# Optimization experiments

Measured on AMD Instinct MI355X. Metric: run time of the kernel, lower is better.

## Reference

```python
import jax, jax.numpy as jnp
import numpy as np

DIM = 1024
NUM_HEADS = 16
HEAD_DIM = DIM // NUM_HEADS
ROPE_THETA = 10000.0


def rms_norm(x, w):
    # torch nn.RMSNorm with eps=None uses finfo(dtype).eps
    eps = jnp.finfo(x.dtype).eps
    var = jnp.mean(jnp.square(x), axis=-1, keepdims=True)
    return x * jax.lax.rsqrt(var + eps) * w


def rope(x, pos, theta=ROPE_THETA):
    # x: (b, h, n, d), pos: (b, n) float positions. Rotate-half RoPE.
    d = x.shape[-1]
    inv_freq = theta ** (-jnp.arange(0, d, 2, dtype=x.dtype) / d)  # (d/2,)
    ang = pos[:, None, :, None] * inv_freq  # (b, 1, n, d/2)
    cos, sin = jnp.cos(ang), jnp.sin(ang)
    x1, x2 = jnp.split(x, 2, axis=-1)
    return jnp.concatenate([x1 * cos - x2 * sin, x1 * sin + x2 * cos], axis=-1)


def setup_inputs() -> dict:
    key = jax.random.key(0)
    ks = jax.random.split(key, 9)
    b, n = 2, 2048
    s = DIM ** -0.5
    return {
        "tgt": jax.random.normal(ks[0], (b, n, DIM), jnp.float32),
        "src": jax.random.normal(ks[1], (b, n, DIM), jnp.float32),
        "tgt_pos": jax.random.uniform(ks[2], (b, n), jnp.float32) * n,
        "src_pos": jax.random.uniform(ks[3], (b, n), jnp.float32) * n,
        "Wq": jax.random.normal(ks[4], (DIM, DIM), jnp.float32) * s,
        "Wkv": jax.random.normal(ks[5], (DIM, 2 * DIM), jnp.float32) * s,
        "Wo": jax.random.normal(ks[6], (DIM, DIM), jnp.float32) * s,
        "q_norm_w": jnp.ones((HEAD_DIM,), jnp.float32),
        "k_norm_w": jnp.ones((HEAD_DIM,), jnp.float32),
    }


def reference(tgt, src, tgt_pos, src_pos, Wq, Wkv, Wo, q_norm_w, k_norm_w):
    b, n, _ = tgt.shape
    m = src.shape[1]
    h, hd = NUM_HEADS, HEAD_DIM
    # q: (b, h, n, hd)
    q = (tgt @ Wq).reshape(b, n, h, hd).transpose(0, 2, 1, 3)
    # kv layout '(two h d)': split into k and v chunks first
    kv = (src @ Wkv).reshape(b, m, 2, h, hd)
    k = kv[:, :, 0].transpose(0, 2, 1, 3)  # (b, h, m, hd)
    v = kv[:, :, 1].transpose(0, 2, 1, 3)
    q = rms_norm(q, q_norm_w)
    k = rms_norm(k, k_norm_w)
    q = rope(q, tgt_pos)
    k = rope(k, src_pos)
    scores = jnp.einsum("bhnd,bhmd->bhnm", q, k) / (hd ** 0.5)
    attn = jax.nn.softmax(scores, axis=-1)
    x = jnp.einsum("bhnm,bhmd->bhnd", attn, v)
    x = x.transpose(0, 2, 1, 3).reshape(b, n, h * hd)
    return x @ Wo
```

## Files before the change

kernel.cpp:

```cpp
#include <hip/hip_runtime.h>
#include <hip/hip_bf16.h>
#include <stdint.h>

#define DIM 1024
#define NH 16
#define HD 64
#define BATCH 2
#define SEQ 2048
#define ROWS (BATCH*SEQ)
#define NS 2
#define CHUNK (SEQ/NS)
#define NT (CHUNK/64)

typedef __attribute__((ext_vector_type(8))) short bf16x8;
typedef __attribute__((ext_vector_type(4))) float f32x4;
typedef __attribute__((ext_vector_type(16))) float f32x16;
typedef __attribute__((ext_vector_type(4))) unsigned short u16x4;
typedef __attribute__((ext_vector_type(4))) unsigned int u32x4;

static __device__ __forceinline__ unsigned short f2bf(float f) {
    union { float f; uint32_t u; } v; v.f = f;
    uint32_t u = v.u;
    uint32_t rnd = 0x7fffu + ((u >> 16) & 1u);
    return (unsigned short)((u + rnd) >> 16);
}

static __device__ __forceinline__ unsigned cvt_pk_bf16(float lo, float hi) {
    unsigned r;
    asm("v_cvt_pk_bf16_f32 %0, %1, %2" : "=v"(r) : "v"(lo), "v"(hi));
    return r;
}

__global__ void k_pre(const float* __restrict__ tgt, const float* __restrict__ src,
                      unsigned short* __restrict__ tgt_b, unsigned short* __restrict__ src_b,
                      const float* __restrict__ Wq, const float* __restrict__ Wkv,
                      const float* __restrict__ Wo,
                      unsigned short* __restrict__ WqT, unsigned short* __restrict__ WkvT,
                      unsigned short* __restrict__ WoT) {
    __shared__ float tile[32][33];
    int blk = blockIdx.x;
    if (blk < 8192) {
        const float* in = (blk < 4096) ? tgt : src;
        unsigned short* out = (blk < 4096) ? tgt_b : src_b;
        int i = ((blk & 4095) * 256 + threadIdx.x) * 4;
        f32x4 v = *(const f32x4*)(in + i);
        u16x4 o;
        o.x = f2bf(v.x); o.y = f2bf(v.y); o.z = f2bf(v.z); o.w = f2bf(v.w);
        *(u16x4*)(out + i) = o;
        return;
    }
    int bp = blk - 8192;
    int bx = bp & 127, by = bp >> 7;
    const float* W; unsigned short* WT; int N, xb;
    if (bx < 32)      { W = Wq;  WT = WqT;  N = DIM;     xb = bx; }
    else if (bx < 96) { W = Wkv; WT = WkvT; N = 2 * DIM; xb = bx - 32; }
    else              { W = Wo;  WT = WoT;  N = DIM;     xb = bx - 96; }
    const int K = DIM;
    int nt = xb * 32, kt = by * 32;
    int x = threadIdx.x & 31, y = threadIdx.x >> 5;
    #pragma unroll
    for (int i = 0; i < 32; i += 8)
        tile[y + i][x] = W[(size_t)(kt + y + i) * N + nt + x];
    __syncthreads();
    #pragma unroll
    for (int i = 0; i < 32; i += 8)
        WT[(size_t)(nt + y + i) * K + kt + x] = f2bf(tile[x][y + i]);
}

__launch_bounds__(256, 3)
__global__ void k_gemm_qkv(const unsigned short* __restrict__ tgt_b,
                           const unsigned short* __restrict__ src_b,
                           const unsigned short* __restrict__ WqT,
                           const unsigned short* __restrict__ WkvT,
                           const float* __restrict__ tpos, const float* __restrict__ spos,
                           const float* __restrict__ qw, const float* __restrict__ kw,
                           unsigned short* __restrict__ q_a, unsigned short* __restrict__ k_f,
                           unsigned short* __restrict__ v_f) {
    __shared__ __align__(16) unsigned short As[128 * 64];
    __shared__ __align__(16) unsigned short Bs[128 * 64];
    const int tid  = threadIdx.x;
    const int wid  = tid >> 6, lane = tid & 63;
    const int l15  = lane & 15, l4 = lane >> 4;
    const int bx = blockIdx.x;
    const unsigned short* A;  const unsigned short* BT;  int n0;
    if (bx < 8) { A = tgt_b; BT = WqT;  n0 = bx * 128; }
    else        { A = src_b; BT = WkvT; n0 = (bx - 8) * 128; }
    const int K = DIM;
    const int m0 = blockIdx.y * 128;
    const int wr = wid >> 1, wc = wid & 1;
    const int srow = lane >> 3, schunk = lane & 7;

    f32x4 acc[4][4] = {};

    for (int kt = 0; kt < K; kt += 64) {
        #pragma unroll
        for (int t = 0; t < 4; ++t) {
            int r  = (t * 4 + wid) * 8 + srow;
            int ck = schunk ^ (r & 7);
            const unsigned short* ga = A  + (size_t)(m0 + r) * K + kt + ck * 8;
            const unsigned short* gb = BT + (size_t)(n0 + r) * K + kt + ck * 8;
            unsigned short* la = As + (t * 4 + wid) * 512 + lane * 8;
            unsigned short* lb = Bs + (t * 4 + wid) * 512 + lane * 8;
            __builtin_amdgcn_global_load_lds((const __attribute__((address_space(1))) void*)ga,
                                             (__attribute__((address_space(3))) void*)la, 16, 0, 0);
            __builtin_amdgcn_global_load_lds((const __attribute__((address_space(1))) void*)gb,
                                             (__attribute__((address_space(3))) void*)lb, 16, 0, 0);
        }
        __syncthreads();
        #pragma unroll
        for (int k0 = 0; k0 < 2; ++k0) {
            bf16x8 af[4], bfr[4];
            int kk = k0 * 32 + l4 * 8;
            #pragma unroll
            for (int i = 0; i < 4; ++i) {
                int ar = wr * 64 + i * 16 + l15;
                af[i]  = *(const bf16x8*)((const char*)As + ar * 128 + ((kk * 2) ^ ((ar & 7) << 4)));
                int br = wc * 64 + i * 16 + l15;
                bfr[i] = *(const bf16x8*)((const char*)Bs + br * 128 + ((kk * 2) ^ ((br & 7) << 4)));
            }
            #pragma unroll
            for (int i = 0; i < 4; ++i)
                #pragma unroll
                for (int j = 0; j < 4; ++j)
                    acc[i][j] = __builtin_amdgcn_mfma_f32_16x16x32_bf16(af[i], bfr[j], acc[i][j], 0, 0, 0);
        }
        __syncthreads();
    }

    const int colbase = n0 + wc * 64;
    const int mode = (bx < 8) ? 0 : ((colbase < 1024) ? 1 : 2);

    if (mode == 2) {
        const int h = (colbase - 1024) >> 6;
        #pragma unroll
        for (int i = 0; i < 4; ++i)
            #pragma unroll
            for (int r = 0; r < 4; ++r) {
                int row = m0 + wr * 64 + i * 16 + l4 * 4 + r;
                int b = row >> 11, mm = row & (SEQ - 1);
                int bh = b * NH + h;
                int t = mm >> 6, ks = (mm >> 5) & 1, kc = (mm >> 4) & 1;
                int hiv = (mm >> 3) & 1, e = mm & 7;
                #pragma unroll
                for (int j = 0; j < 4; ++j) {
                    int dh = j >> 1, l31v = (j & 1) * 16 + l15;
                    size_t idx = (((((size_t)(bh * 32 + t) * 2 + ks) * 2 + kc) * 2 + dh) * 2 + hiv) * 256
                                 + l31v * 8 + e;
                    v_f[idx] = f2bf(acc[i][j][r]);
                }
            }
        return;
    }

    const float* pos = (mode == 0) ? tpos : spos;
    const float* wt  = (mode == 0) ? qw : kw;
    const int h = colbase >> 6;
    const float QS = (mode == 0) ? 0.18033688011112042f : 1.0f;
    const float eps = 1.1920928955078125e-7f;

    float w4[4];
    #pragma unroll
    for (int j = 0; j < 4; ++j) w4[j] = wt[j * 16 + l15];
    float invf0 = __expf(-(float)(2 * l15) * (1.0f / 64.0f) * 9.21034037198f);
    float invf1 = __expf(-(float)(2 * (16 + l15)) * (1.0f / 64.0f) * 9.21034037198f);

    #pragma unroll
    for (int i = 0; i < 4; ++i)
        #pragma unroll
        for (int r = 0; r < 4; ++r) {
            int row = m0 + wr * 64 + i * 16 + l4 * 4 + r;
            float v0 = acc[i][0][r], v1 = acc[i][1][r], v2 = acc[i][2][r], v3 = acc[i][3][r];
            float ssq = v0 * v0 + v1 * v1 + v2 * v2 + v3 * v3;
            ssq += __shfl_xor(ssq, 1, 64);
            ssq += __shfl_xor(ssq, 2, 64);
            ssq += __shfl_xor(ssq, 4, 64);
            ssq += __shfl_xor(ssq, 8, 64);
            float sc = rsqrtf(ssq * (1.0f / 64.0f) + eps);
            v0 *= sc * w4[0]; v1 *= sc * w4[1]; v2 *= sc * w4[2]; v3 *= sc * w4[3];
            float p = pos[row];
            float s0, c0, s1, c1;
            __sincosf(p * invf0, &s0, &c0);
            __sincosf(p * invf1, &s1, &c1);
            float o0 = (v0 * c0 - v2 * s0) * QS;
            float o1 = (v1 * c1 - v3 * s1) * QS;
            float o2 = (v0 * s0 + v2 * c0) * QS;
            float o3 = (v1 * s1 + v3 * c1) * QS;
            int b = row >> 11, n = row & (SEQ - 1);
            if (mode == 0) {
                unsigned short* dst = q_a + ((size_t)(b * NH + h) * SEQ + n) * 64;
                dst[l15]      = f2bf(o0);
                dst[16 + l15] = f2bf(o1);
                dst[32 + l15] = f2bf(o2);
                dst[48 + l15] = f2bf(o3);
            } else {
                int bh = b * NH + h;
                int t = n >> 6, ksn = (n >> 5) & 1, l31k = n & 31;
                int hik = l15 >> 3, e = l15 & 7;
                size_t base = ((size_t)(bh * 32 + t) * 2 + ksn) * 4;
                k_f[(base + 0) * 512 + hik * 256 + l31k * 8 + e] = f2bf(o0);
                k_f[(base + 1) * 512 + hik * 256 + l31k * 8 + e] = f2bf(o1);
                k_f[(base + 2) * 512 + hik * 256 + l31k * 8 + e] = f2bf(o2);
                k_f[(base + 3) * 512 + hik * 256 + l31k * 8 + e] = f2bf(o3);
            }
        }
}

__launch_bounds__(256)
__global__ void k_gemm_bt(const unsigned short* __restrict__ A,
                          const unsigned short* __restrict__ BT,
                          float* __restrict__ C, int M, int N, int K) {
    __shared__ __align__(16) unsigned short As[128 * 64];
    __shared__ __align__(16) unsigned short Bs[128 * 64];
    const int tid  = threadIdx.x;
    const int wid  = tid >> 6, lane = tid & 63;
    const int l15  = lane & 15, l4 = lane >> 4;
    const int m0 = blockIdx.y * 128, n0 = blockIdx.x * 128;
    const int wr = wid >> 1, wc = wid & 1;
    const int srow = lane >> 3, schunk = lane & 7;

    f32x4 acc[4][4] = {};

    for (int kt = 0; kt < K; kt += 64) {
        #pragma unroll
        for (int t = 0; t < 4; ++t) {
            int r  = (t * 4 + wid) * 8 + srow;
            int ck = schunk ^ (r & 7);
            const unsigned short* ga = A  + (size_t)(m0 + r) * K + kt + ck * 8;
            const unsigned short* gb = BT + (size_t)(n0 + r) * K + kt + ck * 8;
            unsigned short* la = As + (t * 4 + wid) * 512 + lane * 8;
            unsigned short* lb = Bs + (t * 4 + wid) * 512 + lane * 8;
            __builtin_amdgcn_global_load_lds((const __attribute__((address_space(1))) void*)ga,
                                             (__attribute__((address_space(3))) void*)la, 16, 0, 0);
            __builtin_amdgcn_global_load_lds((const __attribute__((address_space(1))) void*)gb,
                                             (__attribute__((address_space(3))) void*)lb, 16, 0, 0);
        }
        __syncthreads();
        #pragma unroll
        for (int k0 = 0; k0 < 2; ++k0) {
            bf16x8 af[4], bfr[4];
            int kk = k0 * 32 + l4 * 8;
            #pragma unroll
            for (int i = 0; i < 4; ++i) {
                int ar = wr * 64 + i * 16 + l15;
                af[i]  = *(const bf16x8*)((const char*)As + ar * 128 + ((kk * 2) ^ ((ar & 7) << 4)));
                int br = wc * 64 + i * 16 + l15;
                bfr[i] = *(const bf16x8*)((const char*)Bs + br * 128 + ((kk * 2) ^ ((br & 7) << 4)));
            }
            #pragma unroll
            for (int i = 0; i < 4; ++i)
                #pragma unroll
                for (int j = 0; j < 4; ++j)
                    acc[i][j] = __builtin_amdgcn_mfma_f32_16x16x32_bf16(af[i], bfr[j], acc[i][j], 0, 0, 0);
        }
        __syncthreads();
    }
    #pragma unroll
    for (int i = 0; i < 4; ++i) {
        int rb = m0 + wr * 64 + i * 16 + l4 * 4;
        #pragma unroll
        for (int j = 0; j < 4; ++j) {
            int col = n0 + wc * 64 + j * 16 + l15;
            #pragma unroll
            for (int r = 0; r < 4; ++r)
                C[(size_t)(rb + r) * N + col] = acc[i][j][r];
        }
    }
}

__launch_bounds__(256, 2)
__global__ void k_attn_part(const unsigned short* __restrict__ q_a,
                            const unsigned short* __restrict__ k_f,
                            const unsigned short* __restrict__ v_f,
                            float* __restrict__ o_part, float* __restrict__ ml) {
    const int tid = threadIdx.x;
    const int wid = tid >> 6, lane = tid & 63;
    const int l31 = lane & 31, hi = lane >> 5;
    const int bh = blockIdx.z, ns = blockIdx.y;
    const int q0 = blockIdx.x * 256 + wid * 64;
    const unsigned short* qb = q_a + (size_t)bh * SEQ * 64;

    bf16x8 qfr[2][4];
    #pragma unroll
    for (int qf = 0; qf < 2; ++qf)
        #pragma unroll
        for (int c = 0; c < 4; ++c)
            qfr[qf][c] = *(const bf16x8*)(qb + (size_t)(q0 + qf * 32 + l31) * 64 + c * 16 + hi * 8);

    const bf16x8* kf8 = (const bf16x8*)k_f;
    const bf16x8* vf8 = (const bf16x8*)v_f;

    f32x16 oacc[2][2] = {};
    float lsum[2] = {0.f, 0.f};

    for (int t = 0; t < NT; ++t) {
        const size_t tg = (size_t)bh * 32 + ns * NT + t;
        const bf16x8* kt = kf8 + tg * 512;
        const bf16x8* vt = vf8 + tg * 512;

        bf16x8 kf[2][4];
        #pragma unroll
        for (int ks = 0; ks < 2; ++ks)
            #pragma unroll
            for (int c = 0; c < 4; ++c)
                kf[ks][c] = kt[((ks * 4 + c) * 2 + hi) * 32 + l31];

        f32x16 sacc[2][2] = {};
        #pragma unroll
        for (int ks = 0; ks < 2; ++ks)
            #pragma unroll
            for (int c = 0; c < 4; ++c) {
                sacc[0][ks] = __builtin_amdgcn_mfma_f32_32x32x16_bf16(kf[ks][c], qfr[0][c], sacc[0][ks], 0, 0, 0);
                sacc[1][ks] = __builtin_amdgcn_mfma_f32_32x32x16_bf16(kf[ks][c], qfr[1][c], sacc[1][ks], 0, 0, 0);
            }

        #pragma unroll
        for (int ks = 0; ks < 2; ++ks)
            #pragma unroll
            for (int kc = 0; kc < 2; ++kc) {
                bf16x8 vf[2];
                #pragma unroll
                for (int dh = 0; dh < 2; ++dh)
                    vf[dh] = vt[(((ks * 2 + kc) * 2 + dh) * 2 + hi) * 32 + l31];
                #pragma unroll
                for (int qf = 0; qf < 2; ++qf) {
                    float p[8];
                    #pragma unroll
                    for (int j = 0; j < 8; ++j)
                        p[j] = __builtin_amdgcn_exp2f(sacc[qf][ks][kc * 8 + j]);
                    lsum[qf] += ((p[0] + p[1]) + (p[2] + p[3])) + ((p[4] + p[5]) + (p[6] + p[7]));
                    unsigned a0 = cvt_pk_bf16(p[0], p[1]);
                    unsigned a1 = cvt_pk_bf16(p[2], p[3]);
                    unsigned b0 = cvt_pk_bf16(p[4], p[5]);
                    unsigned b1 = cvt_pk_bf16(p[6], p[7]);
                    asm("v_permlane32_swap_b32 %0, %1" : "+v"(a0), "+v"(b0));
                    asm("v_permlane32_swap_b32 %0, %1" : "+v"(a1), "+v"(b1));
                    u32x4 w; w.x = a0; w.y = a1; w.z = b0; w.w = b1;
                    bf16x8 pa = __builtin_bit_cast(bf16x8, w);
                    #pragma unroll
                    for (int dh = 0; dh < 2; ++dh)
                        oacc[qf][dh] = __builtin_amdgcn_mfma_f32_32x32x16_bf16(pa, vf[dh], oacc[qf][dh], 0, 0, 0);
                }
            }
    }

    lsum[0] += __shfl_xor(lsum[0], 32, 64);
    lsum[1] += __shfl_xor(lsum[1], 32, 64);

    const size_t chunkbase = ((size_t)bh * NS + ns) * SEQ;
    #pragma unroll
    for (int qf = 0; qf < 2; ++qf) {
        #pragma unroll
        for (int r = 0; r < 16; ++r) {
            int qrow = (r & 3) + 8 * (r >> 2) + 4 * hi;
            size_t rowbase = (chunkbase + q0 + qf * 32 + qrow) * 64;
            o_part[rowbase + l31]      = oacc[qf][0][r];
            o_part[rowbase + 32 + l31] = oacc[qf][1][r];
        }
        if (hi == 0)
            ml[chunkbase + q0 + qf * 32 + l31] = lsum[qf];
    }
}

__launch_bounds__(256)
__global__ void k_combine(const float* __restrict__ o_part, const float* __restrict__ ml,
                          unsigned short* __restrict__ xo) {
    int wid = threadIdx.x >> 6, lane = threadIdx.x & 63;
    int idx = blockIdx.x * 4 + wid;
    int bh = idx >> 11, q = idx & (SEQ - 1);
    const size_t base = ((size_t)bh * NS) * SEQ + q;

    float O = 0.f, L = 0.f;
    #pragma unroll
    for (int i = 0; i < NS; ++i) {
        L += ml[base + (size_t)i * SEQ];
        O += o_part[(base + (size_t)i * SEQ) * 64 + lane];
    }
    int b = bh >> 4, h = bh & 15;
    xo[(size_t)(b * SEQ + q) * DIM + h * 64 + lane] = f2bf(O / L);
}

extern "C" void kernel_launch(void* const* d_in, const int* in_sizes, int n_in,
                              void* d_out, int out_size, void* d_ws, size_t ws_size,
                              hipStream_t stream) {
    const float* tgt  = (const float*)d_in[0];
    const float* src  = (const float*)d_in[1];
    const float* tpos = (const float*)d_in[2];
    const float* spos = (const float*)d_in[3];
    const float* Wq   = (const float*)d_in[4];
    const float* Wkv  = (const float*)d_in[5];
    const float* Wo   = (const float*)d_in[6];
    const float* qw   = (const float*)d_in[7];
    const float* kw   = (const float*)d_in[8];
    float* out = (float*)d_out;
    char* ws = (char*)d_ws;

    unsigned short* tgt_b = (unsigned short*)(ws);
    unsigned short* src_b = (unsigned short*)(ws + ( 8u << 20));
    unsigned short* WqT   = (unsigned short*)(ws + (16u << 20));
    unsigned short* WkvT  = (unsigned short*)(ws + (18u << 20));
    unsigned short* WoT   = (unsigned short*)(ws + (22u << 20));
    float*          o_prt = (float*)         (ws + (48u << 20));
    unsigned short* q_a   = (unsigned short*)(ws + (88u << 20));
    unsigned short* k_f   = (unsigned short*)(ws + (96u << 20));
    unsigned short* v_f   = (unsigned short*)(ws + (104u << 20));
    float*          ml    = (float*)         (ws + (112u << 20));
    unsigned short* x_b   = (unsigned short*)(ws);

    k_pre<<<12288, 256, 0, stream>>>(tgt, src, tgt_b, src_b, Wq, Wkv, Wo, WqT, WkvT, WoT);
    k_gemm_qkv<<<dim3(24, 32), 256, 0, stream>>>(tgt_b, src_b, WqT, WkvT,
                                                 tpos, spos, qw, kw, q_a, k_f, v_f);
    k_attn_part<<<dim3(SEQ / 256, NS, BATCH * NH), 256, 0, stream>>>(q_a, k_f, v_f, o_prt, ml);
    k_combine<<<BATCH * NH * SEQ / 4, 256, 0, stream>>>(o_prt, ml, x_b);
    k_gemm_bt<<<dim3( 8, 32), 256, 0, stream>>>(x_b, WoT, out, ROWS, DIM, DIM);
}
```

Baseline: 124.2 us.

## Fuse split-KV combine into attention kernel via shared-memory reduction

The attention kernel now launches 512-thread blocks in which two groups of four waves each process one half of the key sequence for the same query rows. The partial outputs and row sums are merged through shared memory and written directly as bf16, so the separate combine kernel goes away. This removes the fp32 partial-output round trip through global memory and one kernel launch. In exchange the grid has half as many blocks, each larger, and adds block-wide barriers plus about 35 KB of shared memory per block, which may reduce occupancy.

Measured after the change: 116.9 us. 5.9% less time.

```diff
diff --git a/kernel.cpp b/kernel.cpp
--- a/kernel.cpp
+++ b/kernel.cpp
@@ -267,16 +267,18 @@
     }
 }
 
-__launch_bounds__(256, 2)
+__launch_bounds__(512, 2)
 __global__ void k_attn_part(const unsigned short* __restrict__ q_a,
                             const unsigned short* __restrict__ k_f,
                             const unsigned short* __restrict__ v_f,
-                            float* __restrict__ o_part, float* __restrict__ ml) {
+                            unsigned short* __restrict__ x_b) {
+    __shared__ float LO[4][32][68];
     const int tid = threadIdx.x;
     const int wid = tid >> 6, lane = tid & 63;
     const int l31 = lane & 31, hi = lane >> 5;
-    const int bh = blockIdx.z, ns = blockIdx.y;
-    const int q0 = blockIdx.x * 256 + wid * 64;
+    const int pid = wid & 3, ns = wid >> 2;
+    const int bh = blockIdx.y;
+    const int q0 = blockIdx.x * 256 + pid * 64;
     const unsigned short* qb = q_a + (size_t)bh * SEQ * 64;
 
     bf16x8 qfr[2][4];
@@ -286,16 +288,15 @@
         for (int c = 0; c < 4; ++c)
             qfr[qf][c] = *(const bf16x8*)(qb + (size_t)(q0 + qf * 32 + l31) * 64 + c * 16 + hi * 8);
 
-    const bf16x8* kf8 = (const bf16x8*)k_f;
-    const bf16x8* vf8 = (const bf16x8*)v_f;
+    const bf16x8* kf8 = (const bf16x8*)k_f + ((size_t)bh * 32 + ns * NT) * 512;
+    const bf16x8* vf8 = (const bf16x8*)v_f + ((size_t)bh * 32 + ns * NT) * 512;
 
     f32x16 oacc[2][2] = {};
     float lsum[2] = {0.f, 0.f};
 
     for (int t = 0; t < NT; ++t) {
-        const size_t tg = (size_t)bh * 32 + ns * NT + t;
-        const bf16x8* kt = kf8 + tg * 512;
-        const bf16x8* vt = vf8 + tg * 512;
+        const bf16x8* kt = kf8 + (size_t)t * 512;
+        const bf16x8* vt = vf8 + (size_t)t * 512;
 
         bf16x8 kf[2][4];
         #pragma unroll
@@ -346,37 +347,38 @@
     lsum[0] += __shfl_xor(lsum[0], 32, 64);
     lsum[1] += __shfl_xor(lsum[1], 32, 64);
 
-    const size_t chunkbase = ((size_t)bh * NS + ns) * SEQ;
+    if (hi == 0) {
+        LO[pid][l31][64 + ns] = lsum[0];
+        LO[pid][l31][66 + ns] = lsum[1];
+    }
+    const int b_ = bh >> 4, h_ = bh & 15;
     #pragma unroll
     for (int qf = 0; qf < 2; ++qf) {
-        #pragma unroll
-        for (int r = 0; r < 16; ++r) {
-            int qrow = (r & 3) + 8 * (r >> 2) + 4 * hi;
-            size_t rowbase = (chunkbase + q0 + qf * 32 + qrow) * 64;
-            o_part[rowbase + l31]      = oacc[qf][0][r];
-            o_part[rowbase + 32 + l31] = oacc[qf][1][r];
-        }
-        if (hi == 0)
-            ml[chunkbase + q0 + qf * 32 + l31] = lsum[qf];
-    }
-}
-
-__launch_bounds__(256)
-__global__ void k_combine(const float* __restrict__ o_part, const float* __restrict__ ml,
-                          unsigned short* __restrict__ xo) {
-    int wid = threadIdx.x >> 6, lane = threadIdx.x & 63;
-    int idx = blockIdx.x * 4 + wid;
-    int bh = idx >> 11, q = idx & (SEQ - 1);
-    const size_t base = ((size_t)bh * NS) * SEQ + q;
-
-    float O = 0.f, L = 0.f;
-    #pragma unroll
-    for (int i = 0; i < NS; ++i) {
-        L += ml[base + (size_t)i * SEQ];
-        O += o_part[(base + (size_t)i * SEQ) * 64 + lane];
-    }
-    int b = bh >> 4, h = bh & 15;
-    xo[(size_t)(b * SEQ + q) * DIM + h * 64 + lane] = f2bf(O / L);
+        __syncthreads();
+        if (ns == 1) {
+            #pragma unroll
+            for (int r = 0; r < 16; ++r) {
+                int qrow = (r & 3) + 8 * (r >> 2) + 4 * hi;
+                LO[pid][qrow][l31]      = oacc[qf][0][r];
+                LO[pid][qrow][32 + l31] = oacc[qf][1][r];
+            }
+        }
+        __syncthreads();
+        if (ns == 0) {
+            #pragma unroll
+            for (int r = 0; r < 16; ++r) {
+                int qrow = (r & 3) + 8 * (r >> 2) + 4 * hi;
+                float Lt = LO[pid][qrow][64 + 2 * qf] + LO[pid][qrow][65 + 2 * qf];
+                float rec = 1.0f / Lt;
+                float o0 = (oacc[qf][0][r] + LO[pid][qrow][l31])      * rec;
+                float o1 = (oacc[qf][1][r] + LO[pid][qrow][32 + l31]) * rec;
+                int q = q0 + qf * 32 + qrow;
+                unsigned short* dst = x_b + ((size_t)(b_ * SEQ + q)) * DIM + h_ * 64;
+                dst[l31]      = f2bf(o0);
+                dst[32 + l31] = f2bf(o1);
+            }
+        }
+    }
 }
 
 extern "C" void kernel_launch(void* const* d_in, const int* in_sizes, int n_in,
@@ -399,17 +401,14 @@
     unsigned short* WqT   = (unsigned short*)(ws + (16u << 20));
     unsigned short* WkvT  = (unsigned short*)(ws + (18u << 20));
     unsigned short* WoT   = (unsigned short*)(ws + (22u << 20));
-    float*          o_prt = (float*)         (ws + (48u << 20));
     unsigned short* q_a   = (unsigned short*)(ws + (88u << 20));
     unsigned short* k_f   = (unsigned short*)(ws + (96u << 20));
     unsigned short* v_f   = (unsigned short*)(ws + (104u << 20));
-    float*          ml    = (float*)         (ws + (112u << 20));
     unsigned short* x_b   = (unsigned short*)(ws);
 
     k_pre<<<12288, 256, 0, stream>>>(tgt, src, tgt_b, src_b, Wq, Wkv, Wo, WqT, WkvT, WoT);
     k_gemm_qkv<<<dim3(24, 32), 256, 0, stream>>>(tgt_b, src_b, WqT, WkvT,
                                                  tpos, spos, qw, kw, q_a, k_f, v_f);
-    k_attn_part<<<dim3(SEQ / 256, NS, BATCH * NH), 256, 0, stream>>>(q_a, k_f, v_f, o_prt, ml);
-    k_combine<<<BATCH * NH * SEQ / 4, 256, 0, stream>>>(o_prt, ml, x_b);
+    k_attn_part<<<dim3(SEQ / 256, BATCH * NH), 512, 0, stream>>>(q_a, k_f, v_f, x_b);
     k_gemm_bt<<<dim3( 8, 32), 256, 0, stream>>>(x_b, WoT, out, ROWS, DIM, DIM);
 }
```
